# Kernel optimization log

Measured on AMD Instinct MI355X. Metric: run time of the kernel, lower is better.

The kernel has to match this reference:

```python
import jax, jax.numpy as jnp
import numpy as np
from functools import partial

DIVERGENCE_PIVOT = 1.0
MAX_NORM = 10.0
EPS = 1e-8
NORM_EPS = 1e-12  # F.normalize eps
NUM_LAYERS = 6
STRENGTHS = (0.1, 0.1, 0.1)  # entail, contra, neutral

B, DIM = 131072, 256


def _normalize(x, axis=-1):
    n = jnp.linalg.norm(x, axis=axis, keepdims=True)
    return x / jnp.maximum(n, NORM_EPS)


def setup_inputs() -> dict:
    key = jax.random.key(0)
    k0, k1, k2, k3 = jax.random.split(key, 4)
    h0 = jax.random.normal(k0, (B, DIM), dtype=jnp.float32)
    W1 = jax.random.normal(k1, (DIM, DIM), dtype=jnp.float32) * (1.0 / np.sqrt(DIM))
    b1 = jnp.zeros((DIM,), dtype=jnp.float32)
    W2 = jax.random.normal(k2, (DIM, DIM), dtype=jnp.float32) * (1.0 / np.sqrt(DIM))
    b2 = jnp.zeros((DIM,), dtype=jnp.float32)
    anchors = jax.random.normal(k3, (3, DIM), dtype=jnp.float32)  # entail, contra, neutral
    return {"h0": h0, "W1": W1, "b1": b1, "W2": W2, "b2": b2, "anchors": anchors}


def reference(h0, W1, b1, W2, b2, anchors):
    strengths = jnp.asarray(STRENGTHS, dtype=h0.dtype)  # [3]
    a_n = _normalize(anchors)  # [3, D]; anchors passed into step already normalized,
    # and the step's double-normalize of unit vectors is a no-op mathematically.

    def step(h, _):
        h_n = _normalize(h)                       # [B, D]
        align = h_n @ a_n.T                       # [B, 3] cosine alignment
        div = DIVERGENCE_PIVOT - align            # [B, 3]
        # direction = normalize(h - anchor) per anchor
        diff = h[:, None, :] - a_n[None, :, :]    # [B, 3, D]
        direction = _normalize(diff)
        # force_a = -strength_a * div_a * direction_a, summed over anchors
        total_force = -jnp.einsum('a,ba,bad->bd', strengths, div, direction)
        # update MLP: Linear -> tanh -> Linear
        delta = jnp.tanh(h @ W1.T + b1) @ W2.T + b2
        h_new = h + delta + total_force
        n = jnp.linalg.norm(h_new, axis=-1, keepdims=True)
        h_new = jnp.where(n > MAX_NORM, h_new * (MAX_NORM / (n + EPS)), h_new)
        return h_new, (align, div, jnp.abs(div))

    h_final, (aligns, divs, tens) = jax.lax.scan(step, h0, None, length=NUM_LAYERS)
    # traces: [L, B, 3] each (alignment/divergence/tension per anchor per step)
    return h_final, aligns, divs, tens
```

## Files before the change

### kernel.cpp

```cpp
#include <hip/hip_runtime.h>

typedef unsigned short u16;
typedef float    f32x4 __attribute__((ext_vector_type(4)));
typedef short    s16x8 __attribute__((ext_vector_type(8)));
typedef _Float16 f16x8 __attribute__((ext_vector_type(8)));

#define BTOT    131072
#define DIM     256
#define NLAYER  6
#define MROWS   128
#define NTHR    512
#define LSTR    264
#define W2OFF   65536

__device__ __forceinline__ float h2f(u16 u) {
    union { u16 u; _Float16 h; } v; v.u = u; return (float)v.h;
}
__device__ __forceinline__ u16 f2h(float f) {
    union { _Float16 h; u16 u; } v; v.h = (_Float16)f; return v.u;
}
__device__ __forceinline__ float ftanh(float x) {
    float e = __expf(2.0f * x);
    return 1.0f - 2.0f / (e + 1.0f);
}

__global__ void wsplit_kernel(const float* __restrict__ W1, const float* __restrict__ W2,
                              u16* __restrict__ ws) {
    int i = blockIdx.x * 256 + threadIdx.x;
    ws[i]         = f2h(W1[i]);
    ws[W2OFF + i] = f2h(W2[i]);
}

__global__ __launch_bounds__(NTHR) __attribute__((amdgpu_waves_per_eu(2, 2)))
void collapse_kernel(const float* __restrict__ h0,
                     const float* __restrict__ b1g,
                     const float* __restrict__ b2g,
                     const float* __restrict__ ancg,
                     const u16*  __restrict__ ws,
                     float* __restrict__ out)
{
    __shared__ u16   hb_hi[MROWS * LSTR];
    __shared__ u16   hb_lo[MROWS * LSTR];
    __shared__ float dpart[12 * MROWS];
    __shared__ float scal[MROWS * 8];
    __shared__ float anch_inv[3];

    const int t    = threadIdx.x;
    const int w    = t >> 6;
    const int ln   = t & 63;
    const int wr   = w >> 2;
    const int wc   = w & 3;
    const int c15  = ln & 15;
    const int q    = ln >> 4;
    const int wcol = wc << 6;
    const int wrow = wr << 6;
    const int rr   = t >> 2;
    const int ch   = t & 3;
    const long row0 = (long)blockIdx.x * MROWS;

    {
        const f32x4* src = (const f32x4*)(h0 + (row0 + rr) * DIM + (ch << 6));
        u16* dh = hb_hi + rr * LSTR + (ch << 6);
        u16* dl = hb_lo + rr * LSTR + (ch << 6);
        float ss = 0.f;
        #pragma unroll
        for (int j = 0; j < 8; ++j) {
            f32x4 v0 = src[2 * j], v1 = src[2 * j + 1];
            s16x8 vh, vl;
            #pragma unroll
            for (int e = 0; e < 4; ++e) {
                float f = v0[e]; ss = fmaf(f, f, ss);
                u16 hi = f2h(f); vh[e] = (short)hi; vl[e] = (short)f2h(f - h2f(hi));
            }
            #pragma unroll
            for (int e = 0; e < 4; ++e) {
                float f = v1[e]; ss = fmaf(f, f, ss);
                u16 hi = f2h(f); vh[4 + e] = (short)hi; vl[4 + e] = (short)f2h(f - h2f(hi));
            }
            *(s16x8*)(dh + (j << 3)) = vh;
            *(s16x8*)(dl + (j << 3)) = vl;
        }
        ss += __shfl_xor(ss, 1);
        ss += __shfl_xor(ss, 2);
        if (ch == 0) { scal[(rr << 3) + 4] = 1.f; scal[(rr << 3) + 5] = ss; }
    }
    if (w < 3) {
        float ssa = 0.f;
        #pragma unroll
        for (int j = 0; j < 4; ++j) {
            float v = ancg[w * DIM + (ln << 2) + j];
            ssa = fmaf(v, v, ssa);
        }
        #pragma unroll
        for (int m = 1; m < 64; m <<= 1) ssa += __shfl_xor(ssa, m);
        if (ln == 0) anch_inv[w] = 1.f / fmaxf(sqrtf(ssa), 1e-12f);
    }
    __syncthreads();

    f32x4 h[4][4];
    #pragma unroll
    for (int mi = 0; mi < 4; ++mi)
      #pragma unroll
      for (int tn = 0; tn < 4; ++tn)
        #pragma unroll
        for (int rg = 0; rg < 4; ++rg) {
            int off = (wrow + 16 * mi + (q << 2) + rg) * LSTR + wcol + (tn << 4) + c15;
            h[mi][tn][rg] = h2f(hb_hi[off]) + h2f(hb_lo[off]);
        }
    float an[3][4], b1c[4], b2c[4];
    #pragma unroll
    for (int tn = 0; tn < 4; ++tn) {
        int c = wcol + (tn << 4) + c15;
        an[0][tn] = ancg[0 * DIM + c] * anch_inv[0];
        an[1][tn] = ancg[1 * DIM + c] * anch_inv[1];
        an[2][tn] = ancg[2 * DIM + c] * anch_inv[2];
        b1c[tn]   = b1g[c];
        b2c[tn]   = b2g[c];
    }

    const long A0  = (long)BTOT * DIM;
    const long TRL = (long)NLAYER * BTOT * 3;

    auto gemm2 = [&](const u16* wb, f32x4 (&acc)[4][4]) {
        #pragma unroll
        for (int ks = 0; ks < 8; ++ks) {
            f16x8 Ah[4], Al[4];
            #pragma unroll
            for (int mi = 0; mi < 4; ++mi) {
                int off = (wrow + 16 * mi + c15) * LSTR + (ks << 5) + (q << 3);
                Ah[mi] = *(const f16x8*)(hb_hi + off);
                Al[mi] = *(const f16x8*)(hb_lo + off);
            }
            #pragma unroll
            for (int tn = 0; tn < 4; ++tn) {
                const u16* wp = wb + (wcol + (tn << 4) + c15) * 256 + (ks << 5) + (q << 3);
                f16x8 B = *(const f16x8*)wp;
                #pragma unroll
                for (int mi = 0; mi < 4; ++mi) {
                    acc[mi][tn] = __builtin_amdgcn_mfma_f32_16x16x32_f16(Ah[mi], B, acc[mi][tn], 0, 0, 0);
                    acc[mi][tn] = __builtin_amdgcn_mfma_f32_16x16x32_f16(Al[mi], B, acc[mi][tn], 0, 0, 0);
                }
            }
        }
    };

    #pragma unroll 1
    for (int l = 0; l < NLAYER; ++l) {
        f32x4 acc[4][4];
        #pragma unroll
        for (int mi = 0; mi < 4; ++mi)
          #pragma unroll
          for (int tn = 0; tn < 4; ++tn)
            acc[mi][tn] = (f32x4){b1c[tn], b1c[tn], b1c[tn], b1c[tn]};
        gemm2(ws, acc);
        #pragma unroll
        for (int mi = 0; mi < 4; ++mi) {
            #pragma unroll
            for (int rg = 0; rg < 4; ++rg) {
                float p0 = 0.f, p1 = 0.f, p2 = 0.f;
                #pragma unroll
                for (int tn = 0; tn < 4; ++tn) {
                    float hv = h[mi][tn][rg];
                    p0 = fmaf(hv, an[0][tn], p0);
                    p1 = fmaf(hv, an[1][tn], p1);
                    p2 = fmaf(hv, an[2][tn], p2);
                }
                #pragma unroll
                for (int m = 1; m < 16; m <<= 1) {
                    p0 += __shfl_xor(p0, m);
                    p1 += __shfl_xor(p1, m);
                    p2 += __shfl_xor(p2, m);
                }
                if (c15 < 3) {
                    float pv = (c15 == 0) ? p0 : ((c15 == 1) ? p1 : p2);
                    dpart[(wc * 3 + c15) * MROWS + wrow + 16 * mi + (q << 2) + rg] = pv;
                }
            }
        }
        #pragma unroll
        for (int mi = 0; mi < 4; ++mi)
          #pragma unroll
          for (int tn = 0; tn < 4; ++tn)
            #pragma unroll
            for (int rg = 0; rg < 4; ++rg)
              acc[mi][tn][rg] = ftanh(acc[mi][tn][rg]);
        __syncthreads();

        #pragma unroll
        for (int mi = 0; mi < 4; ++mi)
          #pragma unroll
          for (int tn = 0; tn < 4; ++tn)
            #pragma unroll
            for (int rg = 0; rg < 4; ++rg) {
                int off = (wrow + 16 * mi + (q << 2) + rg) * LSTR + wcol + (tn << 4) + c15;
                float zv = acc[mi][tn][rg];
                u16 hi = f2h(zv);
                hb_hi[off] = hi;
                hb_lo[off] = f2h(zv - h2f(hi));
            }
        if (t < MROWS) {
            int r = t;
            float s  = scal[(r << 3) + 4];
            float ss = scal[(r << 3) + 5];
            float rs = 1.f / fmaxf(sqrtf(ss), 1e-12f);
            float cs[3], alpha = 0.f;
            long tb = (long)l * BTOT * 3 + (row0 + r) * 3;
            #pragma unroll
            for (int a = 0; a < 3; ++a) {
                float praw = dpart[(0 * 3 + a) * MROWS + r] + dpart[(1 * 3 + a) * MROWS + r]
                           + dpart[(2 * 3 + a) * MROWS + r] + dpart[(3 * 3 + a) * MROWS + r];
                float d     = s * praw;
                float align = d * rs;
                float div   = 1.f - align;
                float dist  = sqrtf(fmaxf(ss - 2.f * d + 1.f, 0.f));
                float c     = -0.1f * div / fmaxf(dist, 1e-12f);
                cs[a] = c; alpha += c;
                out[A0 + tb + a]           = align;
                out[A0 + TRL + tb + a]     = div;
                out[A0 + 2 * TRL + tb + a] = fabsf(div);
            }
            f32x4 sv = {alpha, cs[0], cs[1], cs[2]};
            *(f32x4*)(scal + (r << 3)) = sv;
        }
        __syncthreads();

        #pragma unroll
        for (int mi = 0; mi < 4; ++mi)
          #pragma unroll
          for (int tn = 0; tn < 4; ++tn)
            acc[mi][tn] = (f32x4){b2c[tn], b2c[tn], b2c[tn], b2c[tn]};
        gemm2(ws + W2OFF, acc);
        #pragma unroll
        for (int mi = 0; mi < 4; ++mi) {
            #pragma unroll
            for (int rg = 0; rg < 4; ++rg) {
                int r = wrow + 16 * mi + (q << 2) + rg;
                f32x4 sv = *(const f32x4*)(scal + (r << 3));
                float s  = scal[(r << 3) + 4];
                float sa = s * (1.f + sv[0]);
                #pragma unroll
                for (int tn = 0; tn < 4; ++tn) {
                    float comb = sv[1] * an[0][tn] + sv[2] * an[1][tn] + sv[3] * an[2][tn];
                    h[mi][tn][rg] = fmaf(sa, h[mi][tn][rg], acc[mi][tn][rg] - comb);
                }
            }
        }
        __syncthreads();

        #pragma unroll
        for (int mi = 0; mi < 4; ++mi)
          #pragma unroll
          for (int tn = 0; tn < 4; ++tn)
            #pragma unroll
            for (int rg = 0; rg < 4; ++rg) {
                int off = (wrow + 16 * mi + (q << 2) + rg) * LSTR + wcol + (tn << 4) + c15;
                float hv = h[mi][tn][rg];
                u16 hi = f2h(hv);
                hb_hi[off] = hi;
                hb_lo[off] = f2h(hv - h2f(hi));
            }
        __syncthreads();

        {
            u16* rh = hb_hi + rr * LSTR + (ch << 6);
            u16* rl = hb_lo + rr * LSTR + (ch << 6);
            float ss = 0.f;
            #pragma unroll
            for (int j = 0; j < 8; ++j) {
                s16x8 vh = *(const s16x8*)(rh + (j << 3));
                s16x8 vl = *(const s16x8*)(rl + (j << 3));
                #pragma unroll
                for (int e = 0; e < 8; ++e) {
                    float f = h2f((u16)vh[e]) + h2f((u16)vl[e]);
                    ss = fmaf(f, f, ss);
                }
            }
            ss += __shfl_xor(ss, 1);
            ss += __shfl_xor(ss, 2);
            float nn = sqrtf(ss);
            float s  = (nn > 10.f) ? (10.f / (nn + 1e-8f)) : 1.f;
            if (ch == 0) { scal[(rr << 3) + 4] = s; scal[(rr << 3) + 5] = ss * s * s; }
            if (s != 1.f) {
                #pragma unroll
                for (int j = 0; j < 8; ++j) {
                    s16x8 vh = *(const s16x8*)(rh + (j << 3));
                    s16x8 vl = *(const s16x8*)(rl + (j << 3));
                    #pragma unroll
                    for (int e = 0; e < 8; ++e) {
                        float f = (h2f((u16)vh[e]) + h2f((u16)vl[e])) * s;
                        u16 hi = f2h(f);
                        vh[e] = (short)hi;
                        vl[e] = (short)f2h(f - h2f(hi));
                    }
                    *(s16x8*)(rh + (j << 3)) = vh;
                    *(s16x8*)(rl + (j << 3)) = vl;
                }
            }
        }
        __syncthreads();
    }

    {
        const u16* sh = hb_hi + rr * LSTR + (ch << 6);
        const u16* sl = hb_lo + rr * LSTR + (ch << 6);
        f32x4* dst = (f32x4*)(out + (row0 + rr) * DIM + (ch << 6));
        #pragma unroll
        for (int j = 0; j < 8; ++j) {
            s16x8 vh = *(const s16x8*)(sh + (j << 3));
            s16x8 vl = *(const s16x8*)(sl + (j << 3));
            f32x4 o0, o1;
            #pragma unroll
            for (int e = 0; e < 4; ++e) o0[e] = h2f((u16)vh[e]) + h2f((u16)vl[e]);
            #pragma unroll
            for (int e = 0; e < 4; ++e) o1[e] = h2f((u16)vh[4 + e]) + h2f((u16)vl[4 + e]);
            dst[2 * j]     = o0;
            dst[2 * j + 1] = o1;
        }
    }
}

extern "C" void kernel_launch(void* const* d_in, const int* in_sizes, int n_in,
                              void* d_out, int out_size, void* d_ws, size_t ws_size,
                              hipStream_t stream) {
    const float* h0 = (const float*)d_in[0];
    const float* W1 = (const float*)d_in[1];
    const float* b1 = (const float*)d_in[2];
    const float* W2 = (const float*)d_in[3];
    const float* b2 = (const float*)d_in[4];
    const float* an = (const float*)d_in[5];
    u16*   ws  = (u16*)d_ws;
    float* out = (float*)d_out;

    wsplit_kernel<<<dim3(DIM * DIM / 256), dim3(256), 0, stream>>>(W1, W2, ws);
    collapse_kernel<<<dim3(BTOT / MROWS), dim3(NTHR), 0, stream>>>(h0, b1, b2, an, ws, out);
}
```

Baseline: 1.409 ms.

## Drop hi/lo fp16 split, fold norm clamp into next layer, convert weights inline

Activations are now held as a single fp16 copy in shared memory instead of a hi+lo pair, which halves the MFMA count and the LDS traffic. The row-norm clamp pass that rescaled shared memory is replaced by per-row partial sums taken from registers, and the scale is applied lazily in the next GEMM epilogue and at output. The separate weight-conversion kernel is removed: fp32 weights are read and cast to fp16 inside the GEMM loop, adding global load bandwidth and conversion work per tile. The cost is precision, since activations keep only fp16 accuracy across six layers.

```diff
diff --git a/kernel.cpp b/kernel.cpp
--- a/kernel.cpp
+++ b/kernel.cpp
@@ -11,7 +11,6 @@
 #define MROWS   128
 #define NTHR    512
 #define LSTR    264
-#define W2OFF   65536
 
 __device__ __forceinline__ float h2f(u16 u) {
     union { u16 u; _Float16 h; } v; v.u = u; return (float)v.h;
@@ -24,24 +23,18 @@
     return 1.0f - 2.0f / (e + 1.0f);
 }
 
-__global__ void wsplit_kernel(const float* __restrict__ W1, const float* __restrict__ W2,
-                              u16* __restrict__ ws) {
-    int i = blockIdx.x * 256 + threadIdx.x;
-    ws[i]         = f2h(W1[i]);
-    ws[W2OFF + i] = f2h(W2[i]);
-}
-
 __global__ __launch_bounds__(NTHR) __attribute__((amdgpu_waves_per_eu(2, 2)))
 void collapse_kernel(const float* __restrict__ h0,
+                     const float* __restrict__ W1g,
                      const float* __restrict__ b1g,
+                     const float* __restrict__ W2g,
                      const float* __restrict__ b2g,
                      const float* __restrict__ ancg,
-                     const u16*  __restrict__ ws,
                      float* __restrict__ out)
 {
-    __shared__ u16   hb_hi[MROWS * LSTR];
-    __shared__ u16   hb_lo[MROWS * LSTR];
+    __shared__ u16   hb[MROWS * LSTR];
     __shared__ float dpart[12 * MROWS];
+    __shared__ float npart[4 * MROWS];
     __shared__ float scal[MROWS * 8];
     __shared__ float anch_inv[3];
 
@@ -60,25 +53,23 @@
 
     {
         const f32x4* src = (const f32x4*)(h0 + (row0 + rr) * DIM + (ch << 6));
-        u16* dh = hb_hi + rr * LSTR + (ch << 6);
-        u16* dl = hb_lo + rr * LSTR + (ch << 6);
+        u16* dh = hb + rr * LSTR + (ch << 6);
         float ss = 0.f;
         #pragma unroll
         for (int j = 0; j < 8; ++j) {
             f32x4 v0 = src[2 * j], v1 = src[2 * j + 1];
-            s16x8 vh, vl;
+            s16x8 vh;
             #pragma unroll
             for (int e = 0; e < 4; ++e) {
-                float f = v0[e]; ss = fmaf(f, f, ss);
-                u16 hi = f2h(f); vh[e] = (short)hi; vl[e] = (short)f2h(f - h2f(hi));
+                u16 hi = f2h(v0[e]); vh[e] = (short)hi;
+                float fq = h2f(hi); ss = fmaf(fq, fq, ss);
             }
             #pragma unroll
             for (int e = 0; e < 4; ++e) {
-                float f = v1[e]; ss = fmaf(f, f, ss);
-                u16 hi = f2h(f); vh[4 + e] = (short)hi; vl[4 + e] = (short)f2h(f - h2f(hi));
+                u16 hi = f2h(v1[e]); vh[4 + e] = (short)hi;
+                float fq = h2f(hi); ss = fmaf(fq, fq, ss);
             }
             *(s16x8*)(dh + (j << 3)) = vh;
-            *(s16x8*)(dl + (j << 3)) = vl;
         }
         ss += __shfl_xor(ss, 1);
         ss += __shfl_xor(ss, 2);
@@ -105,7 +96,7 @@
         #pragma unroll
         for (int rg = 0; rg < 4; ++rg) {
             int off = (wrow + 16 * mi + (q << 2) + rg) * LSTR + wcol + (tn << 4) + c15;
-            h[mi][tn][rg] = h2f(hb_hi[off]) + h2f(hb_lo[off]);
+            h[mi][tn][rg] = h2f(hb[off]);
         }
     float an[3][4], b1c[4], b2c[4];
     #pragma unroll
@@ -121,25 +112,28 @@
     const long A0  = (long)BTOT * DIM;
     const long TRL = (long)NLAYER * BTOT * 3;
 
-    auto gemm2 = [&](const u16* wb, f32x4 (&acc)[4][4]) {
+    auto gemmW = [&](const float* __restrict__ Wg, f32x4 (&acc)[4][4]) {
         #pragma unroll
         for (int ks = 0; ks < 8; ++ks) {
-            f16x8 Ah[4], Al[4];
+            f16x8 A[4];
             #pragma unroll
             for (int mi = 0; mi < 4; ++mi) {
                 int off = (wrow + 16 * mi + c15) * LSTR + (ks << 5) + (q << 3);
-                Ah[mi] = *(const f16x8*)(hb_hi + off);
-                Al[mi] = *(const f16x8*)(hb_lo + off);
+                A[mi] = *(const f16x8*)(hb + off);
             }
             #pragma unroll
             for (int tn = 0; tn < 4; ++tn) {
-                const u16* wp = wb + (wcol + (tn << 4) + c15) * 256 + (ks << 5) + (q << 3);
-                f16x8 B = *(const f16x8*)wp;
-                #pragma unroll
-                for (int mi = 0; mi < 4; ++mi) {
-                    acc[mi][tn] = __builtin_amdgcn_mfma_f32_16x16x32_f16(Ah[mi], B, acc[mi][tn], 0, 0, 0);
-                    acc[mi][tn] = __builtin_amdgcn_mfma_f32_16x16x32_f16(Al[mi], B, acc[mi][tn], 0, 0, 0);
-                }
+                const float* wp = Wg + (wcol + (tn << 4) + c15) * 256 + (ks << 5) + (q << 3);
+                f32x4 w0 = *(const f32x4*)wp;
+                f32x4 w1 = *(const f32x4*)(wp + 4);
+                f16x8 B;
+                #pragma unroll
+                for (int e = 0; e < 4; ++e) B[e]     = (_Float16)w0[e];
+                #pragma unroll
+                for (int e = 0; e < 4; ++e) B[4 + e] = (_Float16)w1[e];
+                #pragma unroll
+                for (int mi = 0; mi < 4; ++mi)
+                    acc[mi][tn] = __builtin_amdgcn_mfma_f32_16x16x32_f16(A[mi], B, acc[mi][tn], 0, 0, 0);
             }
         }
     };
@@ -151,8 +145,8 @@
         for (int mi = 0; mi < 4; ++mi)
           #pragma unroll
           for (int tn = 0; tn < 4; ++tn)
-            acc[mi][tn] = (f32x4){b1c[tn], b1c[tn], b1c[tn], b1c[tn]};
-        gemm2(ws, acc);
+            acc[mi][tn] = (f32x4){0.f, 0.f, 0.f, 0.f};
+        gemmW(W1g, acc);
         #pragma unroll
         for (int mi = 0; mi < 4; ++mi) {
             #pragma unroll
@@ -180,10 +174,12 @@
         #pragma unroll
         for (int mi = 0; mi < 4; ++mi)
           #pragma unroll
-          for (int tn = 0; tn < 4; ++tn)
-            #pragma unroll
-            for (int rg = 0; rg < 4; ++rg)
-              acc[mi][tn][rg] = ftanh(acc[mi][tn][rg]);
+          for (int rg = 0; rg < 4; ++rg) {
+              float s_ = scal[((wrow + 16 * mi + (q << 2) + rg) << 3) + 4];
+              #pragma unroll
+              for (int tn = 0; tn < 4; ++tn)
+                  acc[mi][tn][rg] = ftanh(fmaf(s_, acc[mi][tn][rg], b1c[tn]));
+          }
         __syncthreads();
 
         #pragma unroll
@@ -193,10 +189,7 @@
             #pragma unroll
             for (int rg = 0; rg < 4; ++rg) {
                 int off = (wrow + 16 * mi + (q << 2) + rg) * LSTR + wcol + (tn << 4) + c15;
-                float zv = acc[mi][tn][rg];
-                u16 hi = f2h(zv);
-                hb_hi[off] = hi;
-                hb_lo[off] = f2h(zv - h2f(hi));
+                hb[off] = f2h(acc[mi][tn][rg]);
             }
         if (t < MROWS) {
             int r = t;
@@ -229,7 +222,7 @@
           #pragma unroll
           for (int tn = 0; tn < 4; ++tn)
             acc[mi][tn] = (f32x4){b2c[tn], b2c[tn], b2c[tn], b2c[tn]};
-        gemm2(ws + W2OFF, acc);
+        gemmW(W2g, acc);
         #pragma unroll
         for (int mi = 0; mi < 4; ++mi) {
             #pragma unroll
@@ -238,11 +231,19 @@
                 f32x4 sv = *(const f32x4*)(scal + (r << 3));
                 float s  = scal[(r << 3) + 4];
                 float sa = s * (1.f + sv[0]);
+                float np = 0.f;
                 #pragma unroll
                 for (int tn = 0; tn < 4; ++tn) {
                     float comb = sv[1] * an[0][tn] + sv[2] * an[1][tn] + sv[3] * an[2][tn];
-                    h[mi][tn][rg] = fmaf(sa, h[mi][tn][rg], acc[mi][tn][rg] - comb);
+                    float hv = fmaf(sa, h[mi][tn][rg], acc[mi][tn][rg] - comb);
+                    h[mi][tn][rg] = hv;
+                    np = fmaf(hv, hv, np);
                 }
+                np += __shfl_xor(np, 1);
+                np += __shfl_xor(np, 2);
+                np += __shfl_xor(np, 4);
+                np += __shfl_xor(np, 8);
+                if (c15 == 0) npart[wc * MROWS + r] = np;
             }
         }
         __syncthreads();
@@ -254,65 +255,31 @@
             #pragma unroll
             for (int rg = 0; rg < 4; ++rg) {
                 int off = (wrow + 16 * mi + (q << 2) + rg) * LSTR + wcol + (tn << 4) + c15;
-                float hv = h[mi][tn][rg];
-                u16 hi = f2h(hv);
-                hb_hi[off] = hi;
-                hb_lo[off] = f2h(hv - h2f(hi));
-            }
+                hb[off] = f2h(h[mi][tn][rg]);
+            }
+        if (t < MROWS) {
+            int r = t;
+            float ssr = npart[r] + npart[MROWS + r] + npart[2 * MROWS + r] + npart[3 * MROWS + r];
+            float nn  = sqrtf(ssr);
+            float s   = (nn > 10.f) ? (10.f / (nn + 1e-8f)) : 1.f;
+            scal[(r << 3) + 4] = s;
+            scal[(r << 3) + 5] = ssr * s * s;
+        }
         __syncthreads();
-
-        {
-            u16* rh = hb_hi + rr * LSTR + (ch << 6);
-            u16* rl = hb_lo + rr * LSTR + (ch << 6);
-            float ss = 0.f;
-            #pragma unroll
-            for (int j = 0; j < 8; ++j) {
-                s16x8 vh = *(const s16x8*)(rh + (j << 3));
-                s16x8 vl = *(const s16x8*)(rl + (j << 3));
-                #pragma unroll
-                for (int e = 0; e < 8; ++e) {
-                    float f = h2f((u16)vh[e]) + h2f((u16)vl[e]);
-                    ss = fmaf(f, f, ss);
-                }
-            }
-            ss += __shfl_xor(ss, 1);
-            ss += __shfl_xor(ss, 2);
-            float nn = sqrtf(ss);
-            float s  = (nn > 10.f) ? (10.f / (nn + 1e-8f)) : 1.f;
-            if (ch == 0) { scal[(rr << 3) + 4] = s; scal[(rr << 3) + 5] = ss * s * s; }
-            if (s != 1.f) {
-                #pragma unroll
-                for (int j = 0; j < 8; ++j) {
-                    s16x8 vh = *(const s16x8*)(rh + (j << 3));
-                    s16x8 vl = *(const s16x8*)(rl + (j << 3));
-                    #pragma unroll
-                    for (int e = 0; e < 8; ++e) {
-                        float f = (h2f((u16)vh[e]) + h2f((u16)vl[e])) * s;
-                        u16 hi = f2h(f);
-                        vh[e] = (short)hi;
-                        vl[e] = (short)f2h(f - h2f(hi));
-                    }
-                    *(s16x8*)(rh + (j << 3)) = vh;
-                    *(s16x8*)(rl + (j << 3)) = vl;
-                }
-            }
-        }
-        __syncthreads();
     }
 
     {
-        const u16* sh = hb_hi + rr * LSTR + (ch << 6);
-        const u16* sl = hb_lo + rr * LSTR + (ch << 6);
+        const u16* sh = hb + rr * LSTR + (ch << 6);
+        float s = scal[(rr << 3) + 4];
         f32x4* dst = (f32x4*)(out + (row0 + rr) * DIM + (ch << 6));
         #pragma unroll
         for (int j = 0; j < 8; ++j) {
             s16x8 vh = *(const s16x8*)(sh + (j << 3));
-            s16x8 vl = *(const s16x8*)(sl + (j << 3));
             f32x4 o0, o1;
             #pragma unroll
-            for (int e = 0; e < 4; ++e) o0[e] = h2f((u16)vh[e]) + h2f((u16)vl[e]);
-            #pragma unroll
-            for (int e = 0; e < 4; ++e) o1[e] = h2f((u16)vh[4 + e]) + h2f((u16)vl[4 + e]);
+            for (int e = 0; e < 4; ++e) o0[e] = h2f((u16)vh[e]) * s;
+            #pragma unroll
+            for (int e = 0; e < 4; ++e) o1[e] = h2f((u16)vh[4 + e]) * s;
             dst[2 * j]     = o0;
             dst[2 * j + 1] = o1;
         }
@@ -328,9 +295,8 @@
     const float* W2 = (const float*)d_in[3];
     const float* b2 = (const float*)d_in[4];
     const float* an = (const float*)d_in[5];
-    u16*   ws  = (u16*)d_ws;
     float* out = (float*)d_out;
-
-    wsplit_kernel<<<dim3(DIM * DIM / 256), dim3(256), 0, stream>>>(W1, W2, ws);
-    collapse_kernel<<<dim3(BTOT / MROWS), dim3(NTHR), 0, stream>>>(h0, b1, b2, an, ws, out);
-}
+    (void)d_ws; (void)ws_size;
+
+    collapse_kernel<<<dim3(BTOT / MROWS), dim3(NTHR), 0, stream>>>(h0, W1, b1, W2, b2, an, out);
+}
```

Result: slower. 1.493 ms (+6.0%).
